# Kernel optimization log

Measured on AMD Instinct MI355X. Metric: run time of the kernel, lower is better.

The kernel has to match this reference:

```python
import jax, jax.numpy as jnp
import numpy as np

E, T, K, N = 8, 8192, 2048, 4096  # experts, total tokens, hidden, ffn-out


def setup_inputs() -> dict:
    key = jax.random.key(0)
    k1, k2, k3, k4 = jax.random.split(key, 4)
    a = jax.random.normal(k1, (T, K), dtype=jnp.float32)
    # weight_column_major=True layout: [num_experts, N, K]
    b = jax.random.normal(k2, (E, N, K), dtype=jnp.float32) * 0.02
    c = jnp.zeros((T, N), dtype=jnp.float32)  # preallocated output buffer
    # monotone segment offsets: 0 = p0 <= p1 <= ... <= pE = T
    cuts = jnp.sort(jax.random.randint(k3, (E - 1,), 0, T))
    seg_indptr = jnp.concatenate([
        jnp.zeros((1,), jnp.int64),
        cuts.astype(jnp.int64),
        jnp.full((1,), T, jnp.int64),
    ])
    weight_indices = jax.random.permutation(k4, E).astype(jnp.int64)
    return {
        "a": a,
        "b": b,
        "c": c,
        "batch_size": E,
        "weight_column_major": 1,
        "seg_indptr": seg_indptr,
        "weight_indices": weight_indices,
    }


def reference(a, b, c, batch_size, weight_column_major, seg_indptr, weight_indices):
    # Grouped GEMM: for each segment s, c[p_s:p_{s+1}] = a[p_s:p_{s+1}] @ b[widx[s]].T
    group_sizes = jnp.diff(seg_indptr).astype(jnp.int32)  # [E]
    # gather per-segment weights and convert column-major [E,N,K] -> [E,K,N]
    rhs = jnp.swapaxes(b[weight_indices], 1, 2)
    return jax.lax.ragged_dot(a, rhs, group_sizes)  # [T, N]
```

## Files before the change

### kernel.cpp

```cpp
#include <hip/hip_runtime.h>
#include <stdint.h>
#include <stddef.h>


typedef __attribute__((ext_vector_type(8))) short short8;
typedef __attribute__((ext_vector_type(4))) float floatx4;

constexpr int E_c = 8;
constexpr int T_c = 8192;
constexpr int K_c = 2048;
constexpr int N_c = 4096;
constexpr int BM = 128;
constexpr int BN = 128;
constexpr int BK = 32;
constexpr int KSTEPS = K_c / BK;
constexpr int XTILES = T_c / BM + E_c;
constexpr int YTILES = N_c / BN;

__device__ __forceinline__ uint32_t pack2(float lo, float hi) {
  union { float f; uint32_t u; } a, b;
  a.f = lo; b.f = hi;
  return __builtin_amdgcn_perm(b.u, a.u, 0x07060302u);
}

__global__ __launch_bounds__(256) void cvt_bf16_kernel(
    const float* __restrict__ src, ushort* __restrict__ dst, int n8) {
  int i = blockIdx.x * 256 + threadIdx.x;
  const int stride = gridDim.x * 256;
  for (; i < n8; i += stride) {
    const float4* p = (const float4*)src + (size_t)i * 2;
    float4 v0 = p[0], v1 = p[1];
    int4 o;
    o.x = pack2(v0.x, v0.y);
    o.y = pack2(v0.z, v0.w);
    o.z = pack2(v1.x, v1.y);
    o.w = pack2(v1.z, v1.w);
    ((int4*)dst)[i] = o;
  }
}

__device__ __forceinline__ void gload16(const ushort* g, ushort* l) {
  __builtin_amdgcn_global_load_lds(
      (const __attribute__((address_space(1))) unsigned int*)g,
      (__attribute__((address_space(3))) unsigned int*)l, 16, 0, 0);
}

__global__ __launch_bounds__(256) void grouped_gemm_bf16_kernel(
    const ushort* __restrict__ A, const ushort* __restrict__ B,
    const int* __restrict__ segp, const int* __restrict__ widx,
    float* __restrict__ C) {
  __shared__ ushort As[BM * BK];
  __shared__ ushort Bs[BN * BK];

  const int t = threadIdx.x;

  const int bid = blockIdx.x;
  const int xcd = bid & 7;
  const int i = bid >> 3;
  const int yl = i / XTILES;
  const int x = i - yl * XTILES;
  const int y = xcd * 4 + yl;

  int s = -1, r0i = 0, rendi = 0, acc_t = 0;
#pragma unroll
  for (int e = 0; e < E_c; ++e) {
    int pe = segp[e], pe1 = segp[e + 1];
    int nt = (pe1 - pe + BM - 1) >> 7;
    if (s < 0 && (x - acc_t) < nt) {
      s = e;
      r0i = pe + ((x - acc_t) << 7);
      rendi = pe1;
    }
    acc_t += nt;
  }
  if (s < 0) return;
  const int expert = widx[s];
  const int n0 = y * BN;

  const int wave = t >> 6;
  const int lane = t & 63;
  const int rl = lane >> 2;
  const int kq = lane & 3;

  int ar0 = r0i + wave * 16 + rl;
  int ar1 = ar0 + 64;
  if (ar0 > T_c - 1) ar0 = T_c - 1;
  if (ar1 > T_c - 1) ar1 = T_c - 1;
  const ushort* Ag0 = A + (size_t)ar0 * K_c + kq * 8;
  const ushort* Ag1 = A + (size_t)ar1 * K_c + kq * 8;
  const ushort* Bg0 =
      B + ((size_t)expert * N_c + n0 + wave * 16 + rl) * K_c + kq * 8;
  const ushort* Bg1 = Bg0 + (size_t)64 * K_c;

  ushort* Al0 = As + wave * 512;
  ushort* Al1 = As + 2048 + wave * 512;
  ushort* Bl0 = Bs + wave * 512;
  ushort* Bl1 = Bs + 2048 + wave * 512;

  const int m16 = lane & 15;
  const int quad = lane >> 4;
  const int wm = (wave & 1) << 6;
  const int wn = (wave >> 1) << 6;
  int ia[4], ib[4];
#pragma unroll
  for (int q = 0; q < 4; ++q) {
    ia[q] = (wm + q * 16 + m16) * BK + quad * 8;
    ib[q] = (wn + q * 16 + m16) * BK + quad * 8;
  }

  floatx4 acc[4][4];
#pragma unroll
  for (int p = 0; p < 4; ++p)
#pragma unroll
    for (int q = 0; q < 4; ++q) acc[p][q] = (floatx4){0.f, 0.f, 0.f, 0.f};

#pragma unroll 1
  for (int kt = 0; kt < KSTEPS; ++kt) {
    __syncthreads();
    gload16(Ag0, Al0);
    gload16(Ag1, Al1);
    gload16(Bg0, Bl0);
    gload16(Bg1, Bl1);
    Ag0 += BK; Ag1 += BK; Bg0 += BK; Bg1 += BK;
    __syncthreads();

    short8 aF[4], bF[4];
#pragma unroll
    for (int q = 0; q < 4; ++q) {
      aF[q] = *(const short8*)&As[ia[q]];
      bF[q] = *(const short8*)&Bs[ib[q]];
    }
#pragma unroll
    for (int p = 0; p < 4; ++p)
#pragma unroll
      for (int q = 0; q < 4; ++q)
        acc[p][q] = __builtin_amdgcn_mfma_f32_16x16x32_bf16(aF[p], bF[q],
                                                            acc[p][q], 0, 0, 0);
  }

#pragma unroll
  for (int p = 0; p < 4; ++p) {
    int growb = r0i + wm + p * 16 + quad * 4;
#pragma unroll
    for (int q = 0; q < 4; ++q) {
      int gcol = n0 + wn + q * 16 + m16;
#pragma unroll
      for (int rr = 0; rr < 4; ++rr) {
        int grow = growb + rr;
        if (grow < rendi) C[(size_t)grow * N_c + gcol] = acc[p][q][rr];
      }
    }
  }
}

constexpr int LSTR = 5;

__device__ __forceinline__ void cvt16(const float4* p, int4* c0, int4* c1) {
  c0->x = pack2(p[0].x, p[0].y); c0->y = pack2(p[0].z, p[0].w);
  c0->z = pack2(p[1].x, p[1].y); c0->w = pack2(p[1].z, p[1].w);
  c1->x = pack2(p[2].x, p[2].y); c1->y = pack2(p[2].z, p[2].w);
  c1->z = pack2(p[3].x, p[3].y); c1->w = pack2(p[3].z, p[3].w);
}

__global__ __launch_bounds__(256) void grouped_gemm_fallback(
    const float* __restrict__ A, const float* __restrict__ B,
    const int* __restrict__ segp, const int* __restrict__ widx,
    float* __restrict__ C) {
  __shared__ int4 As[BM * LSTR];
  __shared__ int4 Bs[BN * LSTR];

  const int t = threadIdx.x;
  const int bid = blockIdx.x;
  const int xcd = bid & 7;
  const int i = bid >> 3;
  const int yl = i / XTILES;
  const int x = i - yl * XTILES;
  const int y = xcd * 4 + yl;

  int s = -1, r0i = 0, rendi = 0, acc_t = 0;
#pragma unroll
  for (int e = 0; e < E_c; ++e) {
    int pe = segp[e], pe1 = segp[e + 1];
    int nt = (pe1 - pe + BM - 1) >> 7;
    if (s < 0 && (x - acc_t) < nt) {
      s = e;
      r0i = pe + ((x - acc_t) << 7);
      rendi = pe1;
    }
    acc_t += nt;
  }
  if (s < 0) return;
  const int expert = widx[s];
  const int n0 = y * BN;

  const int r = t >> 1;
  const int h = t & 1;
  int arow = r0i + r;
  if (arow > T_c - 1) arow = T_c - 1;
  const float* Abase = A + (size_t)arow * K_c + h * 16;
  const float* Bbase = B + ((size_t)expert * N_c + n0 + r) * K_c + h * 16;
  const int wI = r * LSTR + 2 * h;

  const int lane = t & 63;
  const int wave = t >> 6;
  const int m16 = lane & 15;
  const int quad = lane >> 4;
  const int wm = (wave & 1) << 6;
  const int wn = (wave >> 1) << 6;
  int ia[4], ib[4];
#pragma unroll
  for (int q = 0; q < 4; ++q) {
    ia[q] = (wm + q * 16 + m16) * LSTR + quad;
    ib[q] = (wn + q * 16 + m16) * LSTR + quad;
  }

  floatx4 acc[4][4];
#pragma unroll
  for (int p = 0; p < 4; ++p)
#pragma unroll
    for (int q = 0; q < 4; ++q) acc[p][q] = (floatx4){0.f, 0.f, 0.f, 0.f};

  float4 pa[4], pb[4];
#pragma unroll
  for (int j = 0; j < 4; ++j) {
    pa[j] = ((const float4*)Abase)[j];
    pb[j] = ((const float4*)Bbase)[j];
  }

#pragma unroll 1
  for (int kt = 0; kt < KSTEPS * BK / 32; ++kt) {
    __syncthreads();
    int4 a0, a1, b0, b1;
    cvt16(pa, &a0, &a1);
    cvt16(pb, &b0, &b1);
    As[wI] = a0; As[wI + 1] = a1;
    Bs[wI] = b0; Bs[wI + 1] = b1;
    __syncthreads();

    const int knext = (kt + 1 < 64) ? kt + 1 : 63;
    const float* an = Abase + knext * 32;
    const float* bn = Bbase + knext * 32;
#pragma unroll
    for (int j = 0; j < 4; ++j) {
      pa[j] = ((const float4*)an)[j];
      pb[j] = ((const float4*)bn)[j];
    }

    short8 aF[4], bF[4];
#pragma unroll
    for (int q = 0; q < 4; ++q) {
      aF[q] = *(const short8*)&As[ia[q]];
      bF[q] = *(const short8*)&Bs[ib[q]];
    }
#pragma unroll
    for (int p = 0; p < 4; ++p)
#pragma unroll
      for (int q = 0; q < 4; ++q)
        acc[p][q] = __builtin_amdgcn_mfma_f32_16x16x32_bf16(aF[p], bF[q],
                                                            acc[p][q], 0, 0, 0);
  }

#pragma unroll
  for (int p = 0; p < 4; ++p) {
    int growb = r0i + wm + p * 16 + quad * 4;
#pragma unroll
    for (int q = 0; q < 4; ++q) {
      int gcol = n0 + wn + q * 16 + m16;
#pragma unroll
      for (int rr = 0; rr < 4; ++rr) {
        int grow = growb + rr;
        if (grow < rendi) C[(size_t)grow * N_c + gcol] = acc[p][q][rr];
      }
    }
  }
}

extern "C" void kernel_launch(void* const* d_in, const int* in_sizes, int n_in,
                              void* d_out, int out_size, void* d_ws, size_t ws_size,
                              hipStream_t stream) {
  const float* A = (const float*)d_in[0];
  const float* B = (const float*)d_in[1];
  const int* segp = (const int*)d_in[5];
  const int* widx = (const int*)d_in[6];
  float* C = (float*)d_out;

  const size_t abytes = (size_t)T_c * K_c * 2;
  const size_t bbytes = (size_t)E_c * N_c * K_c * 2;

  if (ws_size >= abytes + bbytes) {
    ushort* Abf = (ushort*)d_ws;
    ushort* Bbf = Abf + (size_t)T_c * K_c;
    cvt_bf16_kernel<<<2048, 256, 0, stream>>>(A, Abf, T_c * K_c / 8);
    cvt_bf16_kernel<<<2048, 256, 0, stream>>>(B, Bbf, E_c * N_c * K_c / 8);
    grouped_gemm_bf16_kernel<<<dim3(XTILES * YTILES), 256, 0, stream>>>(
        Abf, Bbf, segp, widx, C);
  } else {
    grouped_gemm_fallback<<<dim3(XTILES * YTILES), 256, 0, stream>>>(
        A, B, segp, widx, C);
  }
}
```

Measured before the change: 723.1 us.

## Triple-buffer LDS pipeline with swizzled layout and merge conversion kernels

Replaces the single-buffered load-sync-compute loop of the bf16 grouped GEMM with a three-stage LDS ring, so global-to-LDS loads for step k+2 are issued while step k computes. Synchronisation uses partial vmcnt waits plus raw barriers instead of two __syncthreads per step. A XOR swizzle on the K-chunk offset is added to cut LDS bank conflicts on fragment reads, and MFMA sections are bracketed with s_setprio. The two fp32-to-bf16 conversion launches become one kernel that covers A and B contiguously. The cost is triple the LDS footprint, which may reduce occupancy, plus more delicate wait-count logic.

```diff
diff --git a/kernel.cpp b/kernel.cpp
--- a/kernel.cpp
+++ b/kernel.cpp
@@ -23,18 +23,20 @@
   return __builtin_amdgcn_perm(b.u, a.u, 0x07060302u);
 }
 
-__global__ __launch_bounds__(256) void cvt_bf16_kernel(
-    const float* __restrict__ src, ushort* __restrict__ dst, int n8) {
+__global__ __launch_bounds__(256) void cvt_both_kernel(
+    const float* __restrict__ A, const float* __restrict__ Bm,
+    ushort* __restrict__ dst) {
+  const int n8A = T_c * K_c / 8;
+  const int n8T = n8A + E_c * N_c * K_c / 8;
   int i = blockIdx.x * 256 + threadIdx.x;
   const int stride = gridDim.x * 256;
-  for (; i < n8; i += stride) {
-    const float4* p = (const float4*)src + (size_t)i * 2;
-    float4 v0 = p[0], v1 = p[1];
+  for (; i < n8T; i += stride) {
+    const float* s =
+        (i < n8A) ? A + (size_t)i * 8 : Bm + (size_t)(i - n8A) * 8;
+    float4 v0 = ((const float4*)s)[0], v1 = ((const float4*)s)[1];
     int4 o;
-    o.x = pack2(v0.x, v0.y);
-    o.y = pack2(v0.z, v0.w);
-    o.z = pack2(v1.x, v1.y);
-    o.w = pack2(v1.z, v1.w);
+    o.x = pack2(v0.x, v0.y); o.y = pack2(v0.z, v0.w);
+    o.z = pack2(v1.x, v1.y); o.w = pack2(v1.z, v1.w);
     ((int4*)dst)[i] = o;
   }
 }
@@ -49,8 +51,8 @@
     const ushort* __restrict__ A, const ushort* __restrict__ B,
     const int* __restrict__ segp, const int* __restrict__ widx,
     float* __restrict__ C) {
-  __shared__ ushort As[BM * BK];
-  __shared__ ushort Bs[BN * BK];
+  __shared__ ushort As0[BM * BK], As1[BM * BK], As2[BM * BK];
+  __shared__ ushort Bs0[BN * BK], Bs1[BN * BK], Bs2[BN * BK];
 
   const int t = threadIdx.x;
 
@@ -78,34 +80,29 @@
   const int n0 = y * BN;
 
   const int wave = t >> 6;
-  const int lane = t & 63;
-  const int rl = lane >> 2;
-  const int kq = lane & 3;
-
-  int ar0 = r0i + wave * 16 + rl;
+  const int gc = (((t & 3) ^ ((t >> 3) & 3)) << 3);
+  int ar0 = r0i + (t >> 2);
   int ar1 = ar0 + 64;
   if (ar0 > T_c - 1) ar0 = T_c - 1;
   if (ar1 > T_c - 1) ar1 = T_c - 1;
-  const ushort* Ag0 = A + (size_t)ar0 * K_c + kq * 8;
-  const ushort* Ag1 = A + (size_t)ar1 * K_c + kq * 8;
-  const ushort* Bg0 =
-      B + ((size_t)expert * N_c + n0 + wave * 16 + rl) * K_c + kq * 8;
+  const ushort* Ag0 = A + (size_t)ar0 * K_c + gc;
+  const ushort* Ag1 = A + (size_t)ar1 * K_c + gc;
+  const ushort* Bg0 = B + ((size_t)expert * N_c + n0 + (t >> 2)) * K_c + gc;
   const ushort* Bg1 = Bg0 + (size_t)64 * K_c;
-
-  ushort* Al0 = As + wave * 512;
-  ushort* Al1 = As + 2048 + wave * 512;
-  ushort* Bl0 = Bs + wave * 512;
-  ushort* Bl1 = Bs + 2048 + wave * 512;
-
+  const int lo0 = wave * 512;
+  const int lo1 = 2048 + wave * 512;
+
+  const int lane = t & 63;
   const int m16 = lane & 15;
   const int quad = lane >> 4;
+  const int csw = (quad ^ ((m16 >> 1) & 3)) << 3;
   const int wm = (wave & 1) << 6;
   const int wn = (wave >> 1) << 6;
   int ia[4], ib[4];
 #pragma unroll
   for (int q = 0; q < 4; ++q) {
-    ia[q] = (wm + q * 16 + m16) * BK + quad * 8;
-    ib[q] = (wn + q * 16 + m16) * BK + quad * 8;
+    ia[q] = (wm + q * 16 + m16) * BK + csw;
+    ib[q] = (wn + q * 16 + m16) * BK + csw;
   }
 
   floatx4 acc[4][4];
@@ -114,29 +111,56 @@
 #pragma unroll
     for (int q = 0; q < 4; ++q) acc[p][q] = (floatx4){0.f, 0.f, 0.f, 0.f};
 
+#define STAGE(Asb, Bsb, kc)                                              \
+  {                                                                      \
+    const int ko = (kc)*BK;                                              \
+    gload16(Ag0 + ko, (Asb) + lo0);                                      \
+    gload16(Ag1 + ko, (Asb) + lo1);                                      \
+    gload16(Bg0 + ko, (Bsb) + lo0);                                      \
+    gload16(Bg1 + ko, (Bsb) + lo1);                                      \
+  }
+
+#define COMPUTE(Asb, Bsb)                                                \
+  {                                                                      \
+    short8 aF[4], bF[4];                                                 \
+    _Pragma("unroll") for (int q = 0; q < 4; ++q) {                      \
+      aF[q] = *(const short8*)&(Asb)[ia[q]];                             \
+      bF[q] = *(const short8*)&(Bsb)[ib[q]];                             \
+    }                                                                    \
+    __builtin_amdgcn_s_setprio(1);                                       \
+    _Pragma("unroll") for (int p = 0; p < 4; ++p)                        \
+        _Pragma("unroll") for (int q = 0; q < 4; ++q) acc[p][q] =        \
+        __builtin_amdgcn_mfma_f32_16x16x32_bf16(aF[p], bF[q], acc[p][q], \
+                                                0, 0, 0);                \
+    __builtin_amdgcn_s_setprio(0);                                       \
+  }
+
+#define STEPBAR()                                                        \
+  asm volatile("s_waitcnt vmcnt(4) lgkmcnt(0)" ::: "memory");            \
+  __builtin_amdgcn_s_barrier();
+
+  STAGE(As0, Bs0, 0);
+  STAGE(As1, Bs1, 1);
+  asm volatile("s_waitcnt vmcnt(4)" ::: "memory");
+  __builtin_amdgcn_s_barrier();
+
 #pragma unroll 1
-  for (int kt = 0; kt < KSTEPS; ++kt) {
-    __syncthreads();
-    gload16(Ag0, Al0);
-    gload16(Ag1, Al1);
-    gload16(Bg0, Bl0);
-    gload16(Bg1, Bl1);
-    Ag0 += BK; Ag1 += BK; Bg0 += BK; Bg1 += BK;
-    __syncthreads();
-
-    short8 aF[4], bF[4];
-#pragma unroll
-    for (int q = 0; q < 4; ++q) {
-      aF[q] = *(const short8*)&As[ia[q]];
-      bF[q] = *(const short8*)&Bs[ib[q]];
-    }
-#pragma unroll
-    for (int p = 0; p < 4; ++p)
-#pragma unroll
-      for (int q = 0; q < 4; ++q)
-        acc[p][q] = __builtin_amdgcn_mfma_f32_16x16x32_bf16(aF[p], bF[q],
-                                                            acc[p][q], 0, 0, 0);
-  }
+  for (int k = 0; k < KSTEPS - 1; k += 3) {
+    STAGE(As2, Bs2, k + 2);
+    COMPUTE(As0, Bs0);
+    STEPBAR();
+    STAGE(As0, Bs0, (k + 3 < KSTEPS) ? k + 3 : KSTEPS - 1);
+    COMPUTE(As1, Bs1);
+    STEPBAR();
+    STAGE(As1, Bs1, (k + 4 < KSTEPS) ? k + 4 : KSTEPS - 1);
+    COMPUTE(As2, Bs2);
+    STEPBAR();
+  }
+  COMPUTE(As0, Bs0);
+
+#undef STAGE
+#undef COMPUTE
+#undef STEPBAR
 
 #pragma unroll
   for (int p = 0; p < 4; ++p) {
@@ -228,7 +252,7 @@
   }
 
 #pragma unroll 1
-  for (int kt = 0; kt < KSTEPS * BK / 32; ++kt) {
+  for (int kt = 0; kt < 64; ++kt) {
     __syncthreads();
     int4 a0, a1, b0, b1;
     cvt16(pa, &a0, &a1);
@@ -290,8 +314,7 @@
   if (ws_size >= abytes + bbytes) {
     ushort* Abf = (ushort*)d_ws;
     ushort* Bbf = Abf + (size_t)T_c * K_c;
-    cvt_bf16_kernel<<<2048, 256, 0, stream>>>(A, Abf, T_c * K_c / 8);
-    cvt_bf16_kernel<<<2048, 256, 0, stream>>>(B, Bbf, E_c * N_c * K_c / 8);
+    cvt_both_kernel<<<2048, 256, 0, stream>>>(A, B, Abf);
     grouped_gemm_bf16_kernel<<<dim3(XTILES * YTILES), 256, 0, stream>>>(
         Abf, Bbf, segp, widx, C);
   } else {
```

Measured after the change: 725.1 us. Within noise of the previous version (+0.3%).
